# Performance work log

Measured on AMD Instinct MI355X. Metric: run time of the kernel, lower is better.

The kernel has to match this reference:

```python
import jax, jax.numpy as jnp
import numpy as np

B, C, H, W = 4, 64, 128, 128
HEADS, DIM_HEAD = 8, 64
INNER = HEADS * DIM_HEAD
EPS = 1e-12  # torch F.normalize default eps


def setup_inputs() -> dict:
    key = jax.random.key(0)
    ks = jax.random.split(key, 6)
    s_in = 1.0 / np.sqrt(C)
    s_pr = 1.0 / np.sqrt(INNER)
    return {
        "x_in": jax.random.normal(ks[0], (B, C, H, W), dtype=jnp.float32),
        "Wq": jax.random.uniform(ks[1], (C, INNER), jnp.float32, -s_in, s_in),
        "Wk": jax.random.uniform(ks[2], (C, INNER), jnp.float32, -s_in, s_in),
        "Wv": jax.random.uniform(ks[3], (C, INNER), jnp.float32, -s_in, s_in),
        "Wp": jax.random.uniform(ks[4], (INNER, C), jnp.float32, -s_pr, s_pr),
        "bp": jax.random.uniform(ks[5], (C,), jnp.float32, -s_pr, s_pr),
        "rescale": jnp.ones((HEADS, 1, 1), dtype=jnp.float32),
    }


def _l2norm(t):
    # normalize along last axis (the token axis n), matching F.normalize(p=2)
    n = jnp.sqrt(jnp.sum(t * t, axis=-1, keepdims=True))
    return t / jnp.maximum(n, EPS)


def reference(x_in, Wq, Wk, Wv, Wp, bp, rescale):
    b, c, h, w = x_in.shape
    n = h * w
    x = x_in.transpose(0, 2, 3, 1).reshape(b, n, c)  # [b, n, c]

    def heads_first(t):  # [b, n, inner] -> [b, heads, d, n]
        return t.reshape(b, n, HEADS, DIM_HEAD).transpose(0, 2, 3, 1)

    q = _l2norm(heads_first(x @ Wq))  # [b, H, d, n]
    k = _l2norm(heads_first(x @ Wk))
    v = heads_first(x @ Wv)

    # channel-channel attention: attn[d, e] = sum_n k[d, n] * q[e, n]
    attn = jnp.einsum('bhdn,bhen->bhde', k, q) * rescale  # [b, H, d, d]
    attn = jax.nn.softmax(attn, axis=-1)

    o = jnp.einsum('bhde,bhen->bhdn', attn, v)            # [b, H, d, n]
    o = o.transpose(0, 3, 1, 2).reshape(b, n, INNER)      # [b, n, inner]
    out = (o @ Wp + bp).reshape(b, h, w, c).transpose(0, 3, 1, 2)  # [b, c, h, w]
    return out, attn
```

## Files before the change

kernel.cpp:

```cpp
#include <hip/hip_runtime.h>
#include <math.h>

#define BB 4
#define CC 64
#define NN 16384
#define HEADS 8
#define INNER 512
#define NSLICE 64

__global__ __launch_bounds__(256) void k_gram(const float* __restrict__ x,
                                              float* __restrict__ G) {
    const int s = blockIdx.x, b = blockIdx.y;
    const int t = threadIdx.x;
    const int g = t >> 6, lane = t & 63;
    const int rg = lane >> 4;
    const int r0 = g * 16 + rg * 4;
    const int c0 = (lane & 15) * 4;
    __shared__ float xs[64][68];
    float acc[4][4];
#pragma unroll
    for (int i = 0; i < 4; i++)
#pragma unroll
        for (int j = 0; j < 4; j++) acc[i][j] = 0.f;

    const float* xb = x + (size_t)b * CC * NN;
    const int nbase = s * (NN / NSLICE);
    for (int tile = 0; tile < (NN / NSLICE) / 64; ++tile) {
        const int n0 = nbase + tile * 64;
#pragma unroll
        for (int k = 0; k < 4; k++) {
            int f = k * 256 + t;
            int c = f >> 4, j4 = f & 15;
            const float4 v = *reinterpret_cast<const float4*>(xb + (size_t)c * NN + n0 + j4 * 4);
            xs[j4 * 4 + 0][c] = v.x; xs[j4 * 4 + 1][c] = v.y;
            xs[j4 * 4 + 2][c] = v.z; xs[j4 * 4 + 3][c] = v.w;
        }
        __syncthreads();
#pragma unroll 8
        for (int n = 0; n < 64; ++n) {
            const float4 a4 = *reinterpret_cast<const float4*>(&xs[n][r0]);
            const float4 b4 = *reinterpret_cast<const float4*>(&xs[n][c0]);
            acc[0][0] = fmaf(a4.x, b4.x, acc[0][0]); acc[0][1] = fmaf(a4.x, b4.y, acc[0][1]);
            acc[0][2] = fmaf(a4.x, b4.z, acc[0][2]); acc[0][3] = fmaf(a4.x, b4.w, acc[0][3]);
            acc[1][0] = fmaf(a4.y, b4.x, acc[1][0]); acc[1][1] = fmaf(a4.y, b4.y, acc[1][1]);
            acc[1][2] = fmaf(a4.y, b4.z, acc[1][2]); acc[1][3] = fmaf(a4.y, b4.w, acc[1][3]);
            acc[2][0] = fmaf(a4.z, b4.x, acc[2][0]); acc[2][1] = fmaf(a4.z, b4.y, acc[2][1]);
            acc[2][2] = fmaf(a4.z, b4.z, acc[2][2]); acc[2][3] = fmaf(a4.z, b4.w, acc[2][3]);
            acc[3][0] = fmaf(a4.w, b4.x, acc[3][0]); acc[3][1] = fmaf(a4.w, b4.y, acc[3][1]);
            acc[3][2] = fmaf(a4.w, b4.z, acc[3][2]); acc[3][3] = fmaf(a4.w, b4.w, acc[3][3]);
        }
        __syncthreads();
    }
    float* Gb = G + (size_t)b * 4096;
#pragma unroll
    for (int i = 0; i < 4; i++)
#pragma unroll
        for (int j = 0; j < 4; j++)
            atomicAdd(&Gb[(r0 + i) * 64 + c0 + j], acc[i][j]);
}

__global__ __launch_bounds__(256) void k_attn(const float* __restrict__ G,
                                              const float* __restrict__ Wq,
                                              const float* __restrict__ Wk,
                                              const float* __restrict__ Wv,
                                              const float* __restrict__ Wp,
                                              const float* __restrict__ rescale,
                                              float* __restrict__ attn_out,
                                              float* __restrict__ Mg) {
    const int quad = blockIdx.x & 3;
    const int bh = blockIdx.x >> 2;
    const int b = bh >> 3, h = bh & 7;
    const int d0g = quad * 16;
    const int t = threadIdx.x;

    __shared__ float Gs[64][68];
    __shared__ float Tq[64][68];
    __shared__ float Ws[64][68];
    __shared__ float WkQ[64][20];
    __shared__ float Atn[64][20];
    __shared__ float qn[64], kn[16];

#pragma unroll
    for (int k = 0; k < 4; k++) {
        int idx = k * 1024 + t * 4;
        int r = idx >> 6, c = idx & 63;
        float4 v = *reinterpret_cast<const float4*>(G + (size_t)b * 4096 + idx);
        *reinterpret_cast<float4*>(&Gs[r][c]) = v;
        float4 w = *reinterpret_cast<const float4*>(Wq + (size_t)r * INNER + h * 64 + c);
        *reinterpret_cast<float4*>(&Ws[r][c]) = w;
    }
    {
        int c = t >> 2, dl = (t & 3) * 4;
        float4 v = *reinterpret_cast<const float4*>(Wk + (size_t)c * INNER + h * 64 + d0g + dl);
        *reinterpret_cast<float4*>(&WkQ[c][dl]) = v;
    }
    float4 wvr[4];
#pragma unroll
    for (int k = 0; k < 4; k++) {
        int idx = k * 1024 + t * 4;
        int r = idx >> 6, c = idx & 63;
        wvr[k] = *reinterpret_cast<const float4*>(Wv + (size_t)r * INNER + h * 64 + c);
    }
    float4 wpr;
    {
        int dl = t >> 4, c2 = (t & 15) * 4;
        wpr = *reinterpret_cast<const float4*>(Wp + (size_t)(h * 64 + d0g + dl) * 64 + c2);
    }
    __syncthreads();

    const int ti = t >> 4, tj = t & 15;
    {
        float acc[4][4] = {};
        for (int k2 = 0; k2 < 64; k2++) {
            const float4 a4 = *reinterpret_cast<const float4*>(&Gs[k2][ti * 4]);
            const float4 b4 = *reinterpret_cast<const float4*>(&Ws[k2][tj * 4]);
            float a[4] = {a4.x, a4.y, a4.z, a4.w}, bv[4] = {b4.x, b4.y, b4.z, b4.w};
#pragma unroll
            for (int i = 0; i < 4; i++)
#pragma unroll
                for (int j = 0; j < 4; j++) acc[i][j] = fmaf(a[i], bv[j], acc[i][j]);
        }
#pragma unroll
        for (int i = 0; i < 4; i++) {
            float4 v; v.x = acc[i][0]; v.y = acc[i][1]; v.z = acc[i][2]; v.w = acc[i][3];
            *reinterpret_cast<float4*>(&Tq[ti * 4 + i][tj * 4]) = v;
        }
    }
    {
        const int c = t >> 2, dl0 = (t & 3) * 4;
        float tk[4] = {};
        for (int k = 0; k < 64; k++) {
            const float a = Gs[k][c];
            const float4 b4 = *reinterpret_cast<const float4*>(&WkQ[k][dl0]);
            tk[0] = fmaf(a, b4.x, tk[0]); tk[1] = fmaf(a, b4.y, tk[1]);
            tk[2] = fmaf(a, b4.z, tk[2]); tk[3] = fmaf(a, b4.w, tk[3]);
        }
        float4 v; v.x = tk[0]; v.y = tk[1]; v.z = tk[2]; v.w = tk[3];
        *reinterpret_cast<float4*>(&Atn[c][dl0]) = v;
    }
    __syncthreads();

    {
        const int e = t >> 2, sub = t & 3;
        float s = 0.f;
        for (int c = sub * 16; c < sub * 16 + 16; c++) s += Ws[c][e] * Tq[c][e];
        s += __shfl_xor(s, 1, 64);
        s += __shfl_xor(s, 2, 64);
        if (sub == 0) qn[e] = fmaxf(sqrtf(s), 1e-12f);
    }
    if (t < 64) {
        const int dl = t >> 2, sub = t & 3;
        float s = 0.f;
        for (int c = sub * 16; c < sub * 16 + 16; c++) s += WkQ[c][dl] * Atn[c][dl];
        s += __shfl_xor(s, 1, 64);
        s += __shfl_xor(s, 2, 64);
        if (sub == 0) kn[dl] = fmaxf(sqrtf(s), 1e-12f);
    }
    const int d = t >> 4, e0 = (t & 15) * 4;
    float s4[4] = {};
    for (int c = 0; c < 64; c++) {
        const float a = WkQ[c][d];
        const float4 b4 = *reinterpret_cast<const float4*>(&Tq[c][e0]);
        s4[0] = fmaf(a, b4.x, s4[0]); s4[1] = fmaf(a, b4.y, s4[1]);
        s4[2] = fmaf(a, b4.z, s4[2]); s4[3] = fmaf(a, b4.w, s4[3]);
    }
    __syncthreads();

    const float resc = rescale[h];
    float p[4];
    {
        const float ki = resc / kn[d];
        float m = -3.402823466e+38f;
#pragma unroll
        for (int j = 0; j < 4; j++) {
            p[j] = s4[j] * ki / qn[e0 + j];
            m = fmaxf(m, p[j]);
        }
        for (int o = 1; o < 16; o <<= 1) m = fmaxf(m, __shfl_xor(m, o, 64));
        float ssum = 0.f;
#pragma unroll
        for (int j = 0; j < 4; j++) { p[j] = expf(p[j] - m); ssum += p[j]; }
        for (int o = 1; o < 16; o <<= 1) ssum += __shfl_xor(ssum, o, 64);
        const float inv = 1.f / ssum;
#pragma unroll
        for (int j = 0; j < 4; j++) p[j] *= inv;
    }
    {
        float4 v; v.x = p[0]; v.y = p[1]; v.z = p[2]; v.w = p[3];
        *reinterpret_cast<float4*>(attn_out + (size_t)bh * 4096 + (size_t)(d0g + d) * 64 + e0) = v;
#pragma unroll
        for (int j = 0; j < 4; j++) Atn[e0 + j][d] = p[j];
    }
#pragma unroll
    for (int k = 0; k < 4; k++) {
        int idx = k * 1024 + t * 4;
        int r = idx >> 6, c = idx & 63;
        *reinterpret_cast<float4*>(&Ws[r][c]) = wvr[k];
    }
    {
        int dl = t >> 4, c2 = (t & 15) * 4;
        *reinterpret_cast<float4*>(&Tq[16 + dl][c2]) = wpr;
    }
    __syncthreads();

    {
        const int c = t >> 2, dl0 = (t & 3) * 4;
        float wv4[4] = {};
        for (int e = 0; e < 64; e++) {
            const float a = Ws[c][e];
            const float4 b4 = *reinterpret_cast<const float4*>(&Atn[e][dl0]);
            wv4[0] = fmaf(a, b4.x, wv4[0]); wv4[1] = fmaf(a, b4.y, wv4[1]);
            wv4[2] = fmaf(a, b4.z, wv4[2]); wv4[3] = fmaf(a, b4.w, wv4[3]);
        }
#pragma unroll
        for (int j = 0; j < 4; j++) Tq[dl0 + j][c] = wv4[j];
    }
    __syncthreads();

    {
        float acc[4][4] = {};
#pragma unroll
        for (int dl = 0; dl < 16; dl++) {
            const float4 a4 = *reinterpret_cast<const float4*>(&Tq[dl][ti * 4]);
            const float4 b4 = *reinterpret_cast<const float4*>(&Tq[16 + dl][tj * 4]);
            float a[4] = {a4.x, a4.y, a4.z, a4.w}, bv[4] = {b4.x, b4.y, b4.z, b4.w};
#pragma unroll
            for (int i = 0; i < 4; i++)
#pragma unroll
                for (int j = 0; j < 4; j++) acc[i][j] = fmaf(a[i], bv[j], acc[i][j]);
        }
        float* Mb = Mg + (size_t)b * 4096;
#pragma unroll
        for (int i = 0; i < 4; i++)
#pragma unroll
            for (int j = 0; j < 4; j++)
                atomicAdd(&Mb[(ti * 4 + i) * 64 + tj * 4 + j], acc[i][j]);
    }
}

__global__ __launch_bounds__(256) void k_out(const float* __restrict__ x,
                                             const float* __restrict__ Mg,
                                             const float* __restrict__ bp,
                                             float* __restrict__ out) {
    const int sn = blockIdx.x, b = blockIdx.y;
    const int t = threadIdx.x, ti = t >> 4, tj = t & 15;
    __shared__ float Ms[64][68], xs[64][68];
    for (int k = 0; k < 16; k++) { int f = k * 256 + t; Ms[f >> 6][f & 63] = Mg[(size_t)b * 4096 + f]; }
    const int n0 = sn * 64;
    const float* xb = x + (size_t)b * CC * NN;
#pragma unroll
    for (int k = 0; k < 4; k++) {
        int f = k * 256 + t; int c = f >> 4, j4 = f & 15;
        float4 v = *reinterpret_cast<const float4*>(xb + (size_t)c * NN + n0 + j4 * 4);
        xs[c][j4 * 4 + 0] = v.x; xs[c][j4 * 4 + 1] = v.y;
        xs[c][j4 * 4 + 2] = v.z; xs[c][j4 * 4 + 3] = v.w;
    }
    __syncthreads();
    float acc[4][4];
#pragma unroll
    for (int i = 0; i < 4; i++) {
        const float bv = bp[ti * 4 + i];
#pragma unroll
        for (int j = 0; j < 4; j++) acc[i][j] = bv;
    }
    for (int c = 0; c < 64; c++) {
        const float4 m4 = *reinterpret_cast<const float4*>(&Ms[c][ti * 4]);
        const float4 x4 = *reinterpret_cast<const float4*>(&xs[c][tj * 4]);
        float m[4] = {m4.x, m4.y, m4.z, m4.w}, xv[4] = {x4.x, x4.y, x4.z, x4.w};
#pragma unroll
        for (int i = 0; i < 4; i++)
#pragma unroll
            for (int j = 0; j < 4; j++) acc[i][j] = fmaf(m[i], xv[j], acc[i][j]);
    }
    float* ob = out + (size_t)b * CC * NN;
#pragma unroll
    for (int i = 0; i < 4; i++) {
        float4 v; v.x = acc[i][0]; v.y = acc[i][1]; v.z = acc[i][2]; v.w = acc[i][3];
        *reinterpret_cast<float4*>(ob + (size_t)(ti * 4 + i) * NN + n0 + tj * 4) = v;
    }
}

extern "C" void kernel_launch(void* const* d_in, const int* in_sizes, int n_in,
                              void* d_out, int out_size, void* d_ws, size_t ws_size,
                              hipStream_t stream) {
    const float* x  = (const float*)d_in[0];
    const float* Wq = (const float*)d_in[1];
    const float* Wk = (const float*)d_in[2];
    const float* Wv = (const float*)d_in[3];
    const float* Wp = (const float*)d_in[4];
    const float* bp = (const float*)d_in[5];
    const float* rescale = (const float*)d_in[6];
    float* out = (float*)d_out;
    float* attn_out = out + (size_t)BB * CC * NN;
    float* ws = (float*)d_ws;

    float* G  = ws;
    float* Mg = G + (size_t)BB * 4096;

    hipMemsetAsync(G, 0, (size_t)BB * 4096 * 2 * sizeof(float), stream);
    hipLaunchKernelGGL(k_gram, dim3(NSLICE, BB),      dim3(256), 0, stream, x, G);
    hipLaunchKernelGGL(k_attn, dim3(BB * HEADS * 4),  dim3(256), 0, stream, G, Wq, Wk, Wv, Wp, rescale, attn_out, Mg);
    hipLaunchKernelGGL(k_out,  dim3(NN / 64, BB),     dim3(256), 0, stream, x, Mg, bp, out);
}
```

Baseline: 143.2 us.

## Fuse gram, attention and output kernels into one cooperative persistent kernel

Merges the three kernels into a single cooperative launch of 256 blocks that uses grid-wide syncs between the gram, attention and output-projection phases. The output phase now has each block handle four 64-token tiles instead of launching 1024 blocks, and it reuses the shared-memory buffers. The aim is to remove two kernel launch gaps and the per-kernel ramp and tail. The cost is two grid.sync barriers, fewer blocks during the memory-bound output phase, and only 128 of the 256 blocks doing work in the attention phase.

```diff
diff --git a/kernel.cpp b/kernel.cpp
--- a/kernel.cpp
+++ b/kernel.cpp
@@ -1,282 +1,294 @@
 #include <hip/hip_runtime.h>
+#include <hip/hip_cooperative_groups.h>
 #include <math.h>
+
+namespace cg = cooperative_groups;
 
 #define BB 4
 #define CC 64
 #define NN 16384
 #define HEADS 8
 #define INNER 512
-#define NSLICE 64
-
-__global__ __launch_bounds__(256) void k_gram(const float* __restrict__ x,
-                                              float* __restrict__ G) {
-    const int s = blockIdx.x, b = blockIdx.y;
-    const int t = threadIdx.x;
-    const int g = t >> 6, lane = t & 63;
-    const int rg = lane >> 4;
-    const int r0 = g * 16 + rg * 4;
-    const int c0 = (lane & 15) * 4;
-    __shared__ float xs[64][68];
-    float acc[4][4];
-#pragma unroll
-    for (int i = 0; i < 4; i++)
-#pragma unroll
-        for (int j = 0; j < 4; j++) acc[i][j] = 0.f;
-
-    const float* xb = x + (size_t)b * CC * NN;
-    const int nbase = s * (NN / NSLICE);
-    for (int tile = 0; tile < (NN / NSLICE) / 64; ++tile) {
-        const int n0 = nbase + tile * 64;
-#pragma unroll
-        for (int k = 0; k < 4; k++) {
-            int f = k * 256 + t;
-            int c = f >> 4, j4 = f & 15;
-            const float4 v = *reinterpret_cast<const float4*>(xb + (size_t)c * NN + n0 + j4 * 4);
-            xs[j4 * 4 + 0][c] = v.x; xs[j4 * 4 + 1][c] = v.y;
-            xs[j4 * 4 + 2][c] = v.z; xs[j4 * 4 + 3][c] = v.w;
-        }
-        __syncthreads();
-#pragma unroll 8
-        for (int n = 0; n < 64; ++n) {
-            const float4 a4 = *reinterpret_cast<const float4*>(&xs[n][r0]);
-            const float4 b4 = *reinterpret_cast<const float4*>(&xs[n][c0]);
-            acc[0][0] = fmaf(a4.x, b4.x, acc[0][0]); acc[0][1] = fmaf(a4.x, b4.y, acc[0][1]);
-            acc[0][2] = fmaf(a4.x, b4.z, acc[0][2]); acc[0][3] = fmaf(a4.x, b4.w, acc[0][3]);
-            acc[1][0] = fmaf(a4.y, b4.x, acc[1][0]); acc[1][1] = fmaf(a4.y, b4.y, acc[1][1]);
-            acc[1][2] = fmaf(a4.y, b4.z, acc[1][2]); acc[1][3] = fmaf(a4.y, b4.w, acc[1][3]);
-            acc[2][0] = fmaf(a4.z, b4.x, acc[2][0]); acc[2][1] = fmaf(a4.z, b4.y, acc[2][1]);
-            acc[2][2] = fmaf(a4.z, b4.z, acc[2][2]); acc[2][3] = fmaf(a4.z, b4.w, acc[2][3]);
-            acc[3][0] = fmaf(a4.w, b4.x, acc[3][0]); acc[3][1] = fmaf(a4.w, b4.y, acc[3][1]);
-            acc[3][2] = fmaf(a4.w, b4.z, acc[3][2]); acc[3][3] = fmaf(a4.w, b4.w, acc[3][3]);
-        }
-        __syncthreads();
-    }
-    float* Gb = G + (size_t)b * 4096;
-#pragma unroll
-    for (int i = 0; i < 4; i++)
-#pragma unroll
-        for (int j = 0; j < 4; j++)
-            atomicAdd(&Gb[(r0 + i) * 64 + c0 + j], acc[i][j]);
-}
-
-__global__ __launch_bounds__(256) void k_attn(const float* __restrict__ G,
-                                              const float* __restrict__ Wq,
-                                              const float* __restrict__ Wk,
-                                              const float* __restrict__ Wv,
-                                              const float* __restrict__ Wp,
-                                              const float* __restrict__ rescale,
-                                              float* __restrict__ attn_out,
-                                              float* __restrict__ Mg) {
-    const int quad = blockIdx.x & 3;
-    const int bh = blockIdx.x >> 2;
-    const int b = bh >> 3, h = bh & 7;
-    const int d0g = quad * 16;
-    const int t = threadIdx.x;
-
+
+__global__ __launch_bounds__(256) void k_fused(
+        const float* __restrict__ x,
+        const float* __restrict__ Wq,
+        const float* __restrict__ Wk,
+        const float* __restrict__ Wv,
+        const float* __restrict__ Wp,
+        const float* __restrict__ bp,
+        const float* __restrict__ rescale,
+        float* __restrict__ attn_out,
+        float* __restrict__ G,
+        float* __restrict__ Mg,
+        float* __restrict__ out) {
     __shared__ float Gs[64][68];
     __shared__ float Tq[64][68];
     __shared__ float Ws[64][68];
     __shared__ float WkQ[64][20];
     __shared__ float Atn[64][20];
-    __shared__ float qn[64], kn[16];
-
-#pragma unroll
-    for (int k = 0; k < 4; k++) {
-        int idx = k * 1024 + t * 4;
-        int r = idx >> 6, c = idx & 63;
-        float4 v = *reinterpret_cast<const float4*>(G + (size_t)b * 4096 + idx);
-        *reinterpret_cast<float4*>(&Gs[r][c]) = v;
-        float4 w = *reinterpret_cast<const float4*>(Wq + (size_t)r * INNER + h * 64 + c);
-        *reinterpret_cast<float4*>(&Ws[r][c]) = w;
+    __shared__ float qn[64];
+    __shared__ float kn[16];
+
+    const int bid = blockIdx.x;
+    const int t = threadIdx.x;
+    cg::grid_group grid = cg::this_grid();
+
+    {
+        const int b = bid >> 6, s = bid & 63;
+        const int g = t >> 6, lane = t & 63;
+        const int rg = lane >> 4;
+        const int r0 = g * 16 + rg * 4;
+        const int c0 = (lane & 15) * 4;
+        float acc[4][4];
+#pragma unroll
+        for (int i = 0; i < 4; i++)
+#pragma unroll
+            for (int j = 0; j < 4; j++) acc[i][j] = 0.f;
+
+        const float* xb = x + (size_t)b * CC * NN;
+        const int nbase = s * 256;
+        for (int tile = 0; tile < 4; ++tile) {
+            const int n0 = nbase + tile * 64;
+#pragma unroll
+            for (int k = 0; k < 4; k++) {
+                int f = k * 256 + t;
+                int c = f >> 4, j4 = f & 15;
+                const float4 v = *reinterpret_cast<const float4*>(xb + (size_t)c * NN + n0 + j4 * 4);
+                Gs[j4 * 4 + 0][c] = v.x; Gs[j4 * 4 + 1][c] = v.y;
+                Gs[j4 * 4 + 2][c] = v.z; Gs[j4 * 4 + 3][c] = v.w;
+            }
+            __syncthreads();
+#pragma unroll 8
+            for (int n = 0; n < 64; ++n) {
+                const float4 a4 = *reinterpret_cast<const float4*>(&Gs[n][r0]);
+                const float4 b4 = *reinterpret_cast<const float4*>(&Gs[n][c0]);
+                acc[0][0] = fmaf(a4.x, b4.x, acc[0][0]); acc[0][1] = fmaf(a4.x, b4.y, acc[0][1]);
+                acc[0][2] = fmaf(a4.x, b4.z, acc[0][2]); acc[0][3] = fmaf(a4.x, b4.w, acc[0][3]);
+                acc[1][0] = fmaf(a4.y, b4.x, acc[1][0]); acc[1][1] = fmaf(a4.y, b4.y, acc[1][1]);
+                acc[1][2] = fmaf(a4.y, b4.z, acc[1][2]); acc[1][3] = fmaf(a4.y, b4.w, acc[1][3]);
+                acc[2][0] = fmaf(a4.z, b4.x, acc[2][0]); acc[2][1] = fmaf(a4.z, b4.y, acc[2][1]);
+                acc[2][2] = fmaf(a4.z, b4.z, acc[2][2]); acc[2][3] = fmaf(a4.z, b4.w, acc[2][3]);
+                acc[3][0] = fmaf(a4.w, b4.x, acc[3][0]); acc[3][1] = fmaf(a4.w, b4.y, acc[3][1]);
+                acc[3][2] = fmaf(a4.w, b4.z, acc[3][2]); acc[3][3] = fmaf(a4.w, b4.w, acc[3][3]);
+            }
+            __syncthreads();
+        }
+        float* Gb = G + (size_t)b * 4096;
+#pragma unroll
+        for (int i = 0; i < 4; i++)
+#pragma unroll
+            for (int j = 0; j < 4; j++)
+                atomicAdd(&Gb[(r0 + i) * 64 + c0 + j], acc[i][j]);
     }
+    grid.sync();
+
+    if (bid < 128) {
+        const int quad = bid & 3;
+        const int bh = bid >> 2;
+        const int b = bh >> 3, h = bh & 7;
+        const int d0g = quad * 16;
+
+#pragma unroll
+        for (int k = 0; k < 4; k++) {
+            int idx = k * 1024 + t * 4;
+            int r = idx >> 6, c = idx & 63;
+            float4 v = *reinterpret_cast<const float4*>(G + (size_t)b * 4096 + idx);
+            *reinterpret_cast<float4*>(&Gs[r][c]) = v;
+            float4 w = *reinterpret_cast<const float4*>(Wq + (size_t)r * INNER + h * 64 + c);
+            *reinterpret_cast<float4*>(&Ws[r][c]) = w;
+        }
+        {
+            int c = t >> 2, dl = (t & 3) * 4;
+            float4 v = *reinterpret_cast<const float4*>(Wk + (size_t)c * INNER + h * 64 + d0g + dl);
+            *reinterpret_cast<float4*>(&WkQ[c][dl]) = v;
+        }
+        float4 wvr[4];
+#pragma unroll
+        for (int k = 0; k < 4; k++) {
+            int idx = k * 1024 + t * 4;
+            int r = idx >> 6;
+            wvr[k] = *reinterpret_cast<const float4*>(Wv + (size_t)r * INNER + h * 64 + (idx & 63));
+        }
+        float4 wpr;
+        {
+            int dl = t >> 4, c2 = (t & 15) * 4;
+            wpr = *reinterpret_cast<const float4*>(Wp + (size_t)(h * 64 + d0g + dl) * 64 + c2);
+        }
+        __syncthreads();
+
+        const int ti = t >> 4, tj = t & 15;
+        {
+            float acc[4][4] = {};
+            for (int k2 = 0; k2 < 64; k2++) {
+                const float4 a4 = *reinterpret_cast<const float4*>(&Gs[k2][ti * 4]);
+                const float4 b4 = *reinterpret_cast<const float4*>(&Ws[k2][tj * 4]);
+                float a[4] = {a4.x, a4.y, a4.z, a4.w}, bv[4] = {b4.x, b4.y, b4.z, b4.w};
+#pragma unroll
+                for (int i = 0; i < 4; i++)
+#pragma unroll
+                    for (int j = 0; j < 4; j++) acc[i][j] = fmaf(a[i], bv[j], acc[i][j]);
+            }
+#pragma unroll
+            for (int i = 0; i < 4; i++) {
+                float4 v; v.x = acc[i][0]; v.y = acc[i][1]; v.z = acc[i][2]; v.w = acc[i][3];
+                *reinterpret_cast<float4*>(&Tq[ti * 4 + i][tj * 4]) = v;
+            }
+        }
+        {
+            const int c = t >> 2, dl0 = (t & 3) * 4;
+            float tk[4] = {};
+            for (int k = 0; k < 64; k++) {
+                const float a = Gs[k][c];
+                const float4 b4 = *reinterpret_cast<const float4*>(&WkQ[k][dl0]);
+                tk[0] = fmaf(a, b4.x, tk[0]); tk[1] = fmaf(a, b4.y, tk[1]);
+                tk[2] = fmaf(a, b4.z, tk[2]); tk[3] = fmaf(a, b4.w, tk[3]);
+            }
+            float4 v; v.x = tk[0]; v.y = tk[1]; v.z = tk[2]; v.w = tk[3];
+            *reinterpret_cast<float4*>(&Atn[c][dl0]) = v;
+        }
+        __syncthreads();
+
+        {
+            const int e = t >> 2, sub = t & 3;
+            float s = 0.f;
+            for (int c = sub * 16; c < sub * 16 + 16; c++) s += Ws[c][e] * Tq[c][e];
+            s += __shfl_xor(s, 1, 64);
+            s += __shfl_xor(s, 2, 64);
+            if (sub == 0) qn[e] = fmaxf(sqrtf(s), 1e-12f);
+        }
+        if (t < 64) {
+            const int dl = t >> 2, sub = t & 3;
+            float s = 0.f;
+            for (int c = sub * 16; c < sub * 16 + 16; c++) s += WkQ[c][dl] * Atn[c][dl];
+            s += __shfl_xor(s, 1, 64);
+            s += __shfl_xor(s, 2, 64);
+            if (sub == 0) kn[dl] = fmaxf(sqrtf(s), 1e-12f);
+        }
+        const int d = t >> 4, e0 = (t & 15) * 4;
+        float s4[4] = {};
+        for (int c = 0; c < 64; c++) {
+            const float a = WkQ[c][d];
+            const float4 b4 = *reinterpret_cast<const float4*>(&Tq[c][e0]);
+            s4[0] = fmaf(a, b4.x, s4[0]); s4[1] = fmaf(a, b4.y, s4[1]);
+            s4[2] = fmaf(a, b4.z, s4[2]); s4[3] = fmaf(a, b4.w, s4[3]);
+        }
+        __syncthreads();
+
+        const float resc = rescale[h];
+        float p[4];
+        {
+            const float ki = resc / kn[d];
+            float m = -3.402823466e+38f;
+#pragma unroll
+            for (int j = 0; j < 4; j++) {
+                p[j] = s4[j] * ki / qn[e0 + j];
+                m = fmaxf(m, p[j]);
+            }
+            for (int o = 1; o < 16; o <<= 1) m = fmaxf(m, __shfl_xor(m, o, 64));
+            float ssum = 0.f;
+#pragma unroll
+            for (int j = 0; j < 4; j++) { p[j] = expf(p[j] - m); ssum += p[j]; }
+            for (int o = 1; o < 16; o <<= 1) ssum += __shfl_xor(ssum, o, 64);
+            const float inv = 1.f / ssum;
+#pragma unroll
+            for (int j = 0; j < 4; j++) p[j] *= inv;
+        }
+        {
+            float4 v; v.x = p[0]; v.y = p[1]; v.z = p[2]; v.w = p[3];
+            *reinterpret_cast<float4*>(attn_out + (size_t)bh * 4096 + (size_t)(d0g + d) * 64 + e0) = v;
+#pragma unroll
+            for (int j = 0; j < 4; j++) Atn[e0 + j][d] = p[j];
+        }
+#pragma unroll
+        for (int k = 0; k < 4; k++) {
+            int idx = k * 1024 + t * 4;
+            int r = idx >> 6, c = idx & 63;
+            *reinterpret_cast<float4*>(&Ws[r][c]) = wvr[k];
+        }
+        {
+            int dl = t >> 4, c2 = (t & 15) * 4;
+            *reinterpret_cast<float4*>(&Tq[16 + dl][c2]) = wpr;
+        }
+        __syncthreads();
+
+        {
+            const int c = t >> 2, dl0 = (t & 3) * 4;
+            float wv4[4] = {};
+            for (int e = 0; e < 64; e++) {
+                const float a = Ws[c][e];
+                const float4 b4 = *reinterpret_cast<const float4*>(&Atn[e][dl0]);
+                wv4[0] = fmaf(a, b4.x, wv4[0]); wv4[1] = fmaf(a, b4.y, wv4[1]);
+                wv4[2] = fmaf(a, b4.z, wv4[2]); wv4[3] = fmaf(a, b4.w, wv4[3]);
+            }
+#pragma unroll
+            for (int j = 0; j < 4; j++) Tq[dl0 + j][c] = wv4[j];
+        }
+        __syncthreads();
+
+        {
+            float acc[4][4] = {};
+#pragma unroll
+            for (int dl = 0; dl < 16; dl++) {
+                const float4 a4 = *reinterpret_cast<const float4*>(&Tq[dl][ti * 4]);
+                const float4 b4 = *reinterpret_cast<const float4*>(&Tq[16 + dl][tj * 4]);
+                float a[4] = {a4.x, a4.y, a4.z, a4.w}, bv[4] = {b4.x, b4.y, b4.z, b4.w};
+#pragma unroll
+                for (int i = 0; i < 4; i++)
+#pragma unroll
+                    for (int j = 0; j < 4; j++) acc[i][j] = fmaf(a[i], bv[j], acc[i][j]);
+            }
+            float* Mb = Mg + (size_t)b * 4096;
+#pragma unroll
+            for (int i = 0; i < 4; i++)
+#pragma unroll
+                for (int j = 0; j < 4; j++)
+                    atomicAdd(&Mb[(ti * 4 + i) * 64 + tj * 4 + j], acc[i][j]);
+        }
+    }
+    grid.sync();
+
     {
-        int c = t >> 2, dl = (t & 3) * 4;
-        float4 v = *reinterpret_cast<const float4*>(Wk + (size_t)c * INNER + h * 64 + d0g + dl);
-        *reinterpret_cast<float4*>(&WkQ[c][dl]) = v;
-    }
-    float4 wvr[4];
-#pragma unroll
-    for (int k = 0; k < 4; k++) {
-        int idx = k * 1024 + t * 4;
-        int r = idx >> 6, c = idx & 63;
-        wvr[k] = *reinterpret_cast<const float4*>(Wv + (size_t)r * INNER + h * 64 + c);
-    }
-    float4 wpr;
-    {
-        int dl = t >> 4, c2 = (t & 15) * 4;
-        wpr = *reinterpret_cast<const float4*>(Wp + (size_t)(h * 64 + d0g + dl) * 64 + c2);
-    }
-    __syncthreads();
-
-    const int ti = t >> 4, tj = t & 15;
-    {
-        float acc[4][4] = {};
-        for (int k2 = 0; k2 < 64; k2++) {
-            const float4 a4 = *reinterpret_cast<const float4*>(&Gs[k2][ti * 4]);
-            const float4 b4 = *reinterpret_cast<const float4*>(&Ws[k2][tj * 4]);
-            float a[4] = {a4.x, a4.y, a4.z, a4.w}, bv[4] = {b4.x, b4.y, b4.z, b4.w};
+        const int b = bid >> 6, s2 = bid & 63;
+        const int ti = t >> 4, tj = t & 15;
+        for (int k = 0; k < 16; k++) { int f = k * 256 + t; Ws[f >> 6][f & 63] = Mg[(size_t)b * 4096 + f]; }
+        float bpv[4];
+#pragma unroll
+        for (int i = 0; i < 4; i++) bpv[i] = bp[ti * 4 + i];
+        const float* xb = x + (size_t)b * CC * NN;
+        float* ob = out + (size_t)b * CC * NN;
+#pragma unroll
+        for (int ss = 0; ss < 4; ++ss) {
+            const int n0 = (s2 * 4 + ss) * 64;
+            __syncthreads();
+#pragma unroll
+            for (int k = 0; k < 4; k++) {
+                int f = k * 256 + t; int c = f >> 4, j4 = f & 15;
+                float4 v = *reinterpret_cast<const float4*>(xb + (size_t)c * NN + n0 + j4 * 4);
+                Gs[c][j4 * 4 + 0] = v.x; Gs[c][j4 * 4 + 1] = v.y;
+                Gs[c][j4 * 4 + 2] = v.z; Gs[c][j4 * 4 + 3] = v.w;
+            }
+            __syncthreads();
+            float acc[4][4];
 #pragma unroll
             for (int i = 0; i < 4; i++)
 #pragma unroll
-                for (int j = 0; j < 4; j++) acc[i][j] = fmaf(a[i], bv[j], acc[i][j]);
-        }
-#pragma unroll
-        for (int i = 0; i < 4; i++) {
-            float4 v; v.x = acc[i][0]; v.y = acc[i][1]; v.z = acc[i][2]; v.w = acc[i][3];
-            *reinterpret_cast<float4*>(&Tq[ti * 4 + i][tj * 4]) = v;
-        }
-    }
-    {
-        const int c = t >> 2, dl0 = (t & 3) * 4;
-        float tk[4] = {};
-        for (int k = 0; k < 64; k++) {
-            const float a = Gs[k][c];
-            const float4 b4 = *reinterpret_cast<const float4*>(&WkQ[k][dl0]);
-            tk[0] = fmaf(a, b4.x, tk[0]); tk[1] = fmaf(a, b4.y, tk[1]);
-            tk[2] = fmaf(a, b4.z, tk[2]); tk[3] = fmaf(a, b4.w, tk[3]);
-        }
-        float4 v; v.x = tk[0]; v.y = tk[1]; v.z = tk[2]; v.w = tk[3];
-        *reinterpret_cast<float4*>(&Atn[c][dl0]) = v;
-    }
-    __syncthreads();
-
-    {
-        const int e = t >> 2, sub = t & 3;
-        float s = 0.f;
-        for (int c = sub * 16; c < sub * 16 + 16; c++) s += Ws[c][e] * Tq[c][e];
-        s += __shfl_xor(s, 1, 64);
-        s += __shfl_xor(s, 2, 64);
-        if (sub == 0) qn[e] = fmaxf(sqrtf(s), 1e-12f);
-    }
-    if (t < 64) {
-        const int dl = t >> 2, sub = t & 3;
-        float s = 0.f;
-        for (int c = sub * 16; c < sub * 16 + 16; c++) s += WkQ[c][dl] * Atn[c][dl];
-        s += __shfl_xor(s, 1, 64);
-        s += __shfl_xor(s, 2, 64);
-        if (sub == 0) kn[dl] = fmaxf(sqrtf(s), 1e-12f);
-    }
-    const int d = t >> 4, e0 = (t & 15) * 4;
-    float s4[4] = {};
-    for (int c = 0; c < 64; c++) {
-        const float a = WkQ[c][d];
-        const float4 b4 = *reinterpret_cast<const float4*>(&Tq[c][e0]);
-        s4[0] = fmaf(a, b4.x, s4[0]); s4[1] = fmaf(a, b4.y, s4[1]);
-        s4[2] = fmaf(a, b4.z, s4[2]); s4[3] = fmaf(a, b4.w, s4[3]);
-    }
-    __syncthreads();
-
-    const float resc = rescale[h];
-    float p[4];
-    {
-        const float ki = resc / kn[d];
-        float m = -3.402823466e+38f;
-#pragma unroll
-        for (int j = 0; j < 4; j++) {
-            p[j] = s4[j] * ki / qn[e0 + j];
-            m = fmaxf(m, p[j]);
-        }
-        for (int o = 1; o < 16; o <<= 1) m = fmaxf(m, __shfl_xor(m, o, 64));
-        float ssum = 0.f;
-#pragma unroll
-        for (int j = 0; j < 4; j++) { p[j] = expf(p[j] - m); ssum += p[j]; }
-        for (int o = 1; o < 16; o <<= 1) ssum += __shfl_xor(ssum, o, 64);
-        const float inv = 1.f / ssum;
-#pragma unroll
-        for (int j = 0; j < 4; j++) p[j] *= inv;
-    }
-    {
-        float4 v; v.x = p[0]; v.y = p[1]; v.z = p[2]; v.w = p[3];
-        *reinterpret_cast<float4*>(attn_out + (size_t)bh * 4096 + (size_t)(d0g + d) * 64 + e0) = v;
-#pragma unroll
-        for (int j = 0; j < 4; j++) Atn[e0 + j][d] = p[j];
-    }
-#pragma unroll
-    for (int k = 0; k < 4; k++) {
-        int idx = k * 1024 + t * 4;
-        int r = idx >> 6, c = idx & 63;
-        *reinterpret_cast<float4*>(&Ws[r][c]) = wvr[k];
-    }
-    {
-        int dl = t >> 4, c2 = (t & 15) * 4;
-        *reinterpret_cast<float4*>(&Tq[16 + dl][c2]) = wpr;
-    }
-    __syncthreads();
-
-    {
-        const int c = t >> 2, dl0 = (t & 3) * 4;
-        float wv4[4] = {};
-        for (int e = 0; e < 64; e++) {
-            const float a = Ws[c][e];
-            const float4 b4 = *reinterpret_cast<const float4*>(&Atn[e][dl0]);
-            wv4[0] = fmaf(a, b4.x, wv4[0]); wv4[1] = fmaf(a, b4.y, wv4[1]);
-            wv4[2] = fmaf(a, b4.z, wv4[2]); wv4[3] = fmaf(a, b4.w, wv4[3]);
-        }
-#pragma unroll
-        for (int j = 0; j < 4; j++) Tq[dl0 + j][c] = wv4[j];
-    }
-    __syncthreads();
-
-    {
-        float acc[4][4] = {};
-#pragma unroll
-        for (int dl = 0; dl < 16; dl++) {
-            const float4 a4 = *reinterpret_cast<const float4*>(&Tq[dl][ti * 4]);
-            const float4 b4 = *reinterpret_cast<const float4*>(&Tq[16 + dl][tj * 4]);
-            float a[4] = {a4.x, a4.y, a4.z, a4.w}, bv[4] = {b4.x, b4.y, b4.z, b4.w};
-#pragma unroll
-            for (int i = 0; i < 4; i++)
-#pragma unroll
-                for (int j = 0; j < 4; j++) acc[i][j] = fmaf(a[i], bv[j], acc[i][j]);
-        }
-        float* Mb = Mg + (size_t)b * 4096;
-#pragma unroll
-        for (int i = 0; i < 4; i++)
-#pragma unroll
-            for (int j = 0; j < 4; j++)
-                atomicAdd(&Mb[(ti * 4 + i) * 64 + tj * 4 + j], acc[i][j]);
-    }
-}
-
-__global__ __launch_bounds__(256) void k_out(const float* __restrict__ x,
-                                             const float* __restrict__ Mg,
-                                             const float* __restrict__ bp,
-                                             float* __restrict__ out) {
-    const int sn = blockIdx.x, b = blockIdx.y;
-    const int t = threadIdx.x, ti = t >> 4, tj = t & 15;
-    __shared__ float Ms[64][68], xs[64][68];
-    for (int k = 0; k < 16; k++) { int f = k * 256 + t; Ms[f >> 6][f & 63] = Mg[(size_t)b * 4096 + f]; }
-    const int n0 = sn * 64;
-    const float* xb = x + (size_t)b * CC * NN;
-#pragma unroll
-    for (int k = 0; k < 4; k++) {
-        int f = k * 256 + t; int c = f >> 4, j4 = f & 15;
-        float4 v = *reinterpret_cast<const float4*>(xb + (size_t)c * NN + n0 + j4 * 4);
-        xs[c][j4 * 4 + 0] = v.x; xs[c][j4 * 4 + 1] = v.y;
-        xs[c][j4 * 4 + 2] = v.z; xs[c][j4 * 4 + 3] = v.w;
-    }
-    __syncthreads();
-    float acc[4][4];
-#pragma unroll
-    for (int i = 0; i < 4; i++) {
-        const float bv = bp[ti * 4 + i];
-#pragma unroll
-        for (int j = 0; j < 4; j++) acc[i][j] = bv;
-    }
-    for (int c = 0; c < 64; c++) {
-        const float4 m4 = *reinterpret_cast<const float4*>(&Ms[c][ti * 4]);
-        const float4 x4 = *reinterpret_cast<const float4*>(&xs[c][tj * 4]);
-        float m[4] = {m4.x, m4.y, m4.z, m4.w}, xv[4] = {x4.x, x4.y, x4.z, x4.w};
-#pragma unroll
-        for (int i = 0; i < 4; i++)
-#pragma unroll
-            for (int j = 0; j < 4; j++) acc[i][j] = fmaf(m[i], xv[j], acc[i][j]);
-    }
-    float* ob = out + (size_t)b * CC * NN;
-#pragma unroll
-    for (int i = 0; i < 4; i++) {
-        float4 v; v.x = acc[i][0]; v.y = acc[i][1]; v.z = acc[i][2]; v.w = acc[i][3];
-        *reinterpret_cast<float4*>(ob + (size_t)(ti * 4 + i) * NN + n0 + tj * 4) = v;
+                for (int j = 0; j < 4; j++) acc[i][j] = bpv[i];
+            for (int c = 0; c < 64; c++) {
+                const float4 m4 = *reinterpret_cast<const float4*>(&Ws[c][ti * 4]);
+                const float4 x4 = *reinterpret_cast<const float4*>(&Gs[c][tj * 4]);
+                float m[4] = {m4.x, m4.y, m4.z, m4.w}, xv[4] = {x4.x, x4.y, x4.z, x4.w};
+#pragma unroll
+                for (int i = 0; i < 4; i++)
+#pragma unroll
+                    for (int j = 0; j < 4; j++) acc[i][j] = fmaf(m[i], xv[j], acc[i][j]);
+            }
+#pragma unroll
+            for (int i = 0; i < 4; i++) {
+                float4 v; v.x = acc[i][0]; v.y = acc[i][1]; v.z = acc[i][2]; v.w = acc[i][3];
+                *reinterpret_cast<float4*>(ob + (size_t)(ti * 4 + i) * NN + n0 + tj * 4) = v;
+            }
+        }
     }
 }
 
@@ -298,7 +310,8 @@
     float* Mg = G + (size_t)BB * 4096;
 
     hipMemsetAsync(G, 0, (size_t)BB * 4096 * 2 * sizeof(float), stream);
-    hipLaunchKernelGGL(k_gram, dim3(NSLICE, BB),      dim3(256), 0, stream, x, G);
-    hipLaunchKernelGGL(k_attn, dim3(BB * HEADS * 4),  dim3(256), 0, stream, G, Wq, Wk, Wv, Wp, rescale, attn_out, Mg);
-    hipLaunchKernelGGL(k_out,  dim3(NN / 64, BB),     dim3(256), 0, stream, x, Mg, bp, out);
+    void* args[] = { (void*)&x, (void*)&Wq, (void*)&Wk, (void*)&Wv, (void*)&Wp,
+                     (void*)&bp, (void*)&rescale, (void*)&attn_out,
+                     (void*)&G, (void*)&Mg, (void*)&out };
+    hipLaunchCooperativeKernel((void*)k_fused, dim3(256), dim3(256), args, 0, stream);
 }
```

Result: slower. 213.8 us (+49.3%).

## Replace Gram atomics with per-slice partials plus reduction kernel, raise slice count

Applied to the files above, without the earlier changes.

The Gram kernel now writes per-slice partial 64x64 matrices to workspace instead of atomically adding into G, and a new reduction kernel sums the partials. The slice count goes from 64 up to 256, capped by the workspace size, so more blocks run the Gram pass. The memset is removed and Mg is zeroed inside the Gram kernel by slice 0. This trades atomic contention and the memset for an extra launch and extra partial traffic.

```diff
diff --git a/kernel.cpp b/kernel.cpp
--- a/kernel.cpp
+++ b/kernel.cpp
@@ -6,12 +6,18 @@
 #define NN 16384
 #define HEADS 8
 #define INNER 512
-#define NSLICE 64
 
 __global__ __launch_bounds__(256) void k_gram(const float* __restrict__ x,
-                                              float* __restrict__ G) {
+                                              float* __restrict__ part,
+                                              float* __restrict__ Mg,
+                                              int nslice) {
     const int s = blockIdx.x, b = blockIdx.y;
     const int t = threadIdx.x;
+    if (s == 0) {
+        float* Mb = Mg + (size_t)b * 4096;
+#pragma unroll
+        for (int k = 0; k < 16; k++) Mb[k * 256 + t] = 0.f;
+    }
     const int g = t >> 6, lane = t & 63;
     const int rg = lane >> 4;
     const int r0 = g * 16 + rg * 4;
@@ -24,8 +30,10 @@
         for (int j = 0; j < 4; j++) acc[i][j] = 0.f;
 
     const float* xb = x + (size_t)b * CC * NN;
-    const int nbase = s * (NN / NSLICE);
-    for (int tile = 0; tile < (NN / NSLICE) / 64; ++tile) {
+    const int cols = NN / nslice;
+    const int ntiles = cols >> 6;
+    const int nbase = s * cols;
+    for (int tile = 0; tile < ntiles; ++tile) {
         const int n0 = nbase + tile * 64;
 #pragma unroll
         for (int k = 0; k < 4; k++) {
@@ -51,12 +59,28 @@
         }
         __syncthreads();
     }
-    float* Gb = G + (size_t)b * 4096;
-#pragma unroll
-    for (int i = 0; i < 4; i++)
-#pragma unroll
-        for (int j = 0; j < 4; j++)
-            atomicAdd(&Gb[(r0 + i) * 64 + c0 + j], acc[i][j]);
+    float* p = part + (size_t)(b * nslice + s) * 4096;
+#pragma unroll
+    for (int i = 0; i < 4; i++) {
+        float4 v; v.x = acc[i][0]; v.y = acc[i][1]; v.z = acc[i][2]; v.w = acc[i][3];
+        *reinterpret_cast<float4*>(p + (r0 + i) * 64 + c0) = v;
+    }
+}
+
+__global__ __launch_bounds__(256) void k_redG(const float* __restrict__ part,
+                                              float* __restrict__ G,
+                                              int nslice) {
+    const int b = blockIdx.y;
+    const int idx = blockIdx.x * 256 + threadIdx.x;
+    const float* p = part + (size_t)b * nslice * 4096 + idx;
+    float s0 = 0.f, s1 = 0.f, s2 = 0.f, s3 = 0.f;
+    for (int s = 0; s < nslice; s += 4) {
+        s0 += p[(size_t)s * 4096];
+        s1 += p[(size_t)(s + 1) * 4096];
+        s2 += p[(size_t)(s + 2) * 4096];
+        s3 += p[(size_t)(s + 3) * 4096];
+    }
+    G[(size_t)b * 4096 + idx] = (s0 + s1) + (s2 + s3);
 }
 
 __global__ __launch_bounds__(256) void k_attn(const float* __restrict__ G,
@@ -98,8 +122,8 @@
 #pragma unroll
     for (int k = 0; k < 4; k++) {
         int idx = k * 1024 + t * 4;
-        int r = idx >> 6, c = idx & 63;
-        wvr[k] = *reinterpret_cast<const float4*>(Wv + (size_t)r * INNER + h * 64 + c);
+        int r = idx >> 6;
+        wvr[k] = *reinterpret_cast<const float4*>(Wv + (size_t)r * INNER + h * 64 + (idx & 63));
     }
     float4 wpr;
     {
@@ -294,11 +318,19 @@
     float* attn_out = out + (size_t)BB * CC * NN;
     float* ws = (float*)d_ws;
 
-    float* G  = ws;
-    float* Mg = G + (size_t)BB * 4096;
-
-    hipMemsetAsync(G, 0, (size_t)BB * 4096 * 2 * sizeof(float), stream);
-    hipLaunchKernelGGL(k_gram, dim3(NSLICE, BB),      dim3(256), 0, stream, x, G);
-    hipLaunchKernelGGL(k_attn, dim3(BB * HEADS * 4),  dim3(256), 0, stream, G, Wq, Wk, Wv, Wp, rescale, attn_out, Mg);
-    hipLaunchKernelGGL(k_out,  dim3(NN / 64, BB),     dim3(256), 0, stream, x, Mg, bp, out);
-}
+    const size_t fixed_floats = (size_t)BB * 4096
+                              + (size_t)BB * 4096;
+    int nslice = 256;
+    while (nslice > 4 &&
+           ((size_t)BB * nslice * 4096 + fixed_floats) * sizeof(float) > ws_size)
+        nslice >>= 1;
+
+    float* part = ws;
+    float* G    = part + (size_t)BB * nslice * 4096;
+    float* Mg   = G + (size_t)BB * 4096;
+
+    hipLaunchKernelGGL(k_gram, dim3(nslice, BB),     dim3(256), 0, stream, x, part, Mg, nslice);
+    hipLaunchKernelGGL(k_redG, dim3(16, BB),         dim3(256), 0, stream, part, G, nslice);
+    hipLaunchKernelGGL(k_attn, dim3(BB * HEADS * 4), dim3(256), 0, stream, G, Wq, Wk, Wv, Wp, rescale, attn_out, Mg);
+    hipLaunchKernelGGL(k_out,  dim3(NN / 64, BB),    dim3(256), 0, stream, x, Mg, bp, out);
+}
```

After: 143.0 us. About the same (-0.2%).
